# Kernel optimization log

Measured on AMD Instinct MI355X. Metric: run time of the kernel, lower is better.

Reference implementation:

```python
import jax, jax.numpy as jnp
import numpy as np

N_NODES = 100000
N_EDGES = 600000
HIDDEN = 128
BN_EPS = 1e-5


def setup_inputs() -> dict:
    key = jax.random.key(0)
    k_x, k_e, k_w, k_b, k_g = jax.random.split(key, 5)
    x = jax.random.normal(k_x, (N_NODES, HIDDEN), dtype=jnp.float32)
    edge_index = jax.random.randint(k_e, (2, N_EDGES), 0, N_NODES, dtype=jnp.int64)
    # GCNConv linear weight (no bias on the linear; bias added post-aggregation)
    scale = 1.0 / np.sqrt(HIDDEN)
    W = jax.random.uniform(k_w, (HIDDEN, HIDDEN), jnp.float32, -scale, scale)
    b = jax.random.uniform(k_b, (HIDDEN,), jnp.float32, -scale, scale)
    gamma = jnp.ones((HIDDEN,), jnp.float32)   # BatchNorm weight
    beta = jnp.zeros((HIDDEN,), jnp.float32)   # BatchNorm bias
    return {"x": x, "edge_index": edge_index, "W": W, "b": b, "gamma": gamma, "beta": beta}


def reference(x, edge_index, W, b, gamma, beta):
    N = x.shape[0]
    # ReLU then GCNConv linear transform: [N, D]
    h = jnp.matmul(jax.nn.relu(x), W)
    # Add self-loops (PyG GCNConv default)
    loops = jnp.arange(N, dtype=edge_index.dtype)
    row = jnp.concatenate([edge_index[0], loops])  # source nodes
    col = jnp.concatenate([edge_index[1], loops])  # target nodes
    # Symmetric normalization deg^{-1/2} with unit edge weights
    ones = jnp.ones(row.shape[0], dtype=h.dtype)
    deg = jax.ops.segment_sum(ones, col, num_segments=N)
    dinv = jnp.where(deg > 0, jax.lax.rsqrt(deg), 0.0)
    norm = dinv[row] * dinv[col]  # [E+N]
    # Gather -> scale -> scatter-add aggregation, then conv bias
    agg = jax.ops.segment_sum(norm[:, None] * h[row], col, num_segments=N)
    out = agg + b
    # BatchNorm1d (training mode: batch stats, biased variance)
    mean = jnp.mean(out, axis=0)
    var = jnp.var(out, axis=0)
    return gamma * (out - mean) * jax.lax.rsqrt(var + BN_EPS) + beta
```

## Files before the change

### kernel.cpp

```cpp
#include <hip/hip_runtime.h>

#define D 128
#define CAP 32
#define BN_EPS 1e-5f

typedef float floatx4 __attribute__((ext_vector_type(4)));
typedef __bf16 bf16x8 __attribute__((ext_vector_type(8)));

__device__ inline unsigned short f2bf(float f) {
    unsigned u; __builtin_memcpy(&u, &f, 4);
    unsigned r = (u + 0x7FFFu + ((u >> 16) & 1u)) >> 16;
    return (unsigned short)r;
}
__device__ inline float bflo(unsigned v) { unsigned x = v << 16; float f; __builtin_memcpy(&f, &x, 4); return f; }
__device__ inline float bfhi(unsigned v) { unsigned x = v & 0xFFFF0000u; float f; __builtin_memcpy(&f, &x, 4); return f; }

__global__ void setup_k(const unsigned* __restrict__ e, int* __restrict__ flag,
                        int* __restrict__ cursor, float* __restrict__ sums,
                        float* __restrict__ sumsq, const float* __restrict__ W,
                        unsigned short* __restrict__ Wt, int n_nodes) {
    int i = blockIdx.x * blockDim.x + threadIdx.x;
    if (i < n_nodes) cursor[i] = 0;
    if (i < D) { sums[i] = 0.f; sumsq[i] = 0.f; }
    if (i < D * D) {
        int n = i >> 7, k = i & 127;
        Wt[n * D + k] = f2bf(W[k * D + n]);
    }
    if (i == 0) {
        unsigned acc = 0;
        for (int k = 0; k < 64; ++k) acc |= e[2 * k + 1];
        *flag = (acc == 0u) ? 1 : 0;
    }
}

__global__ __launch_bounds__(256, 2) void gemm_k(const float* __restrict__ x,
                                                 const unsigned short* __restrict__ Wt,
                                                 unsigned short* __restrict__ h,
                                                 int n_mtiles) {
    int lane = threadIdx.x & 63;
    int wave = blockIdx.x * 4 + (threadIdx.x >> 6);
    int nw = gridDim.x * 4;
    int l15 = lane & 15;
    int quad = lane >> 4;

    bf16x8 Bf[4][8];
    for (int ks = 0; ks < 4; ++ks)
        for (int j = 0; j < 8; ++j)
            Bf[ks][j] = *(const bf16x8*)(Wt + (size_t)(j * 16 + l15) * D + ks * 32 + quad * 8);

    for (int mt = wave; mt < n_mtiles; mt += nw) {
        const float* xrow = x + (size_t)(mt * 16 + l15) * D + quad * 8;
        bf16x8 Af[4];
        for (int ks = 0; ks < 4; ++ks) {
            float4 a0 = *(const float4*)(xrow + ks * 32);
            float4 a1 = *(const float4*)(xrow + ks * 32 + 4);
            float av[8] = {a0.x, a0.y, a0.z, a0.w, a1.x, a1.y, a1.z, a1.w};
            union { unsigned short u[8]; bf16x8 v; } tmp;
            for (int jj = 0; jj < 8; ++jj) tmp.u[jj] = f2bf(fmaxf(av[jj], 0.0f));
            Af[ks] = tmp.v;
        }
        floatx4 acc[8];
        for (int j = 0; j < 8; ++j) acc[j] = (floatx4){0.f, 0.f, 0.f, 0.f};
        for (int ks = 0; ks < 4; ++ks)
            for (int j = 0; j < 8; ++j)
                acc[j] = __builtin_amdgcn_mfma_f32_16x16x32_bf16(Af[ks], Bf[ks][j], acc[j], 0, 0, 0);
        for (int j = 0; j < 8; ++j)
            for (int reg = 0; reg < 4; ++reg) {
                int rr = mt * 16 + quad * 4 + reg;
                int cc = j * 16 + l15;
                h[(size_t)rr * D + cc] = f2bf(acc[j][reg]);
            }
    }
}

__global__ __launch_bounds__(256) void bucket_k(const void* __restrict__ ep, const int* __restrict__ flag,
                                                int* __restrict__ cursor, int* __restrict__ bucket,
                                                int n_edges) {
    int e = blockIdx.x * blockDim.x + threadIdx.x;
    if (e >= n_edges) return;
    int r, c;
    if (*flag) {
        const long long* p = (const long long*)ep;
        r = (int)p[e]; c = (int)p[e + n_edges];
    } else {
        const int* p = (const int*)ep;
        r = p[e]; c = p[e + n_edges];
    }
    int pos = atomicAdd(&cursor[c], 1);
    if (pos < CAP) bucket[(size_t)c * CAP + pos] = r;
}

__global__ void dinv_k(const int* __restrict__ cursor, float* __restrict__ dinv, int n_nodes) {
    int i = blockIdx.x * blockDim.x + threadIdx.x;
    if (i < n_nodes) dinv[i] = rsqrtf(1.0f + (float)cursor[i]);
}

#define PREPD(s, rr) { int r_ = ((s) < degc) ? (rr) : node;              \
                       w##s = ((s) < degc) ? dinv[r_] : 0.0f;            \
                       hv##s = hp[(unsigned)r_ * 64u + lane]; }
#define ACC(s) { ax += w##s * bflo(hv##s); ay += w##s * bfhi(hv##s); }

__global__ __launch_bounds__(256) void agg_k(const unsigned short* __restrict__ h,
                                             const int* __restrict__ bucket,
                                             const int* __restrict__ cursor,
                                             const float* __restrict__ dinv,
                                             unsigned* __restrict__ aggb,
                                             int n_nodes) {
    int lane = threadIdx.x & 63;
    int node = blockIdx.x * 4 + (threadIdx.x >> 6);
    if (node >= n_nodes) return;
    const unsigned* hp = (const unsigned*)h;

    int deg = cursor[node];
    int degc = deg < CAP ? deg : CAP;
    float dc = dinv[node];

    unsigned v = hp[(unsigned)node * 64u + lane];
    float ax = dc * bflo(v), ay = dc * bfhi(v);
    const int* bk = bucket + (size_t)node * CAP;

    float w0=0,w1=0,w2=0,w3=0,w4=0,w5=0,w6=0,w7=0;
    unsigned hv0=0,hv1=0,hv2=0,hv3=0,hv4=0,hv5=0,hv6=0,hv7=0;

    if (degc > 0) { int4 b = *(const int4*)(bk);     PREPD(0,b.x) PREPD(1,b.y) PREPD(2,b.z) PREPD(3,b.w) }
    if (degc > 4) { int4 b = *(const int4*)(bk + 4); PREPD(4,b.x) PREPD(5,b.y) PREPD(6,b.z) PREPD(7,b.w) }

    if (degc <= 8) {
        ACC(0) ACC(1) ACC(2) ACC(3) ACC(4) ACC(5) ACC(6) ACC(7)
    } else {
        float w8=0,w9=0,w10=0,w11=0,w12=0,w13=0,w14=0,w15=0;
        unsigned hv8=0,hv9=0,hv10=0,hv11=0,hv12=0,hv13=0,hv14=0,hv15=0;
        { int4 b = *(const int4*)(bk + 8); PREPD(8,b.x) PREPD(9,b.y) PREPD(10,b.z) PREPD(11,b.w) }
        if (degc > 12) { int4 b = *(const int4*)(bk + 12); PREPD(12,b.x) PREPD(13,b.y) PREPD(14,b.z) PREPD(15,b.w) }
        ACC(0)  ACC(1)  ACC(2)  ACC(3)  ACC(4)  ACC(5)  ACC(6)  ACC(7)
        ACC(8)  ACC(9)  ACC(10) ACC(11) ACC(12) ACC(13) ACC(14) ACC(15)
        for (int e = 16; e < degc; ++e) {
            int r = bk[e];
            float dr = dinv[r];
            unsigned hh = hp[(unsigned)r * 64u + lane];
            ax += dr * bflo(hh); ay += dr * bfhi(hh);
        }
    }

    float ox = dc * ax, oy = dc * ay;
    aggb[(unsigned)node * 64u + lane] = ((unsigned)f2bf(oy) << 16) | (unsigned)f2bf(ox);
}

__global__ __launch_bounds__(256) void stats_k(const unsigned* __restrict__ aggb,
                                               float* __restrict__ sums, float* __restrict__ sumsq,
                                               int n_nodes) {
    __shared__ float red[256];
    int lane = threadIdx.x & 63;
    int wib = threadIdx.x >> 6;
    int wave = blockIdx.x * 4 + wib;
    int nw = gridDim.x * 4;
    float s0 = 0.f, s1 = 0.f, q0 = 0.f, q1 = 0.f;
    int n = wave;
    for (; n + 3 * nw < n_nodes; n += 4 * nw) {
        unsigned p0 = aggb[(size_t)n * 64 + lane];
        unsigned p1 = aggb[(size_t)(n + nw) * 64 + lane];
        unsigned p2 = aggb[(size_t)(n + 2 * nw) * 64 + lane];
        unsigned p3 = aggb[(size_t)(n + 3 * nw) * 64 + lane];
        float a0 = bflo(p0), b0 = bfhi(p0), a1 = bflo(p1), b1 = bfhi(p1);
        float a2 = bflo(p2), b2 = bfhi(p2), a3 = bflo(p3), b3 = bfhi(p3);
        s0 += a0 + a1 + a2 + a3;
        s1 += b0 + b1 + b2 + b3;
        q0 += a0 * a0 + a1 * a1 + a2 * a2 + a3 * a3;
        q1 += b0 * b0 + b1 * b1 + b2 * b2 + b3 * b3;
    }
    for (; n < n_nodes; n += nw) {
        unsigned p = aggb[(size_t)n * 64 + lane];
        float vx = bflo(p), vy = bfhi(p);
        s0 += vx; s1 += vy; q0 += vx * vx; q1 += vy * vy;
    }
    red[threadIdx.x] = s0; __syncthreads();
    if (wib == 0) atomicAdd(&sums[2 * lane], red[lane] + red[64 + lane] + red[128 + lane] + red[192 + lane]);
    __syncthreads();
    red[threadIdx.x] = s1; __syncthreads();
    if (wib == 0) atomicAdd(&sums[2 * lane + 1], red[lane] + red[64 + lane] + red[128 + lane] + red[192 + lane]);
    __syncthreads();
    red[threadIdx.x] = q0; __syncthreads();
    if (wib == 0) atomicAdd(&sumsq[2 * lane], red[lane] + red[64 + lane] + red[128 + lane] + red[192 + lane]);
    __syncthreads();
    red[threadIdx.x] = q1; __syncthreads();
    if (wib == 0) atomicAdd(&sumsq[2 * lane + 1], red[lane] + red[64 + lane] + red[128 + lane] + red[192 + lane]);
}

__global__ __launch_bounds__(256) void final_k(const unsigned* __restrict__ aggb,
                                               const float* __restrict__ sums, const float* __restrict__ sumsq,
                                               const float* __restrict__ gamma, const float* __restrict__ beta,
                                               float* __restrict__ out, int total4, float inv_n) {
    int i = blockIdx.x * blockDim.x + threadIdx.x;
    if (i >= total4) return;
    int idx = i * 4;
    int f = idx & (D - 1);
    float4 sm = *(const float4*)(sums + f);
    float4 sq = *(const float4*)(sumsq + f);
    float4 g  = *(const float4*)(gamma + f);
    float4 bt = *(const float4*)(beta + f);
    uint2 p = *(const uint2*)(aggb + i * 2);

    float m0 = sm.x * inv_n, m1 = sm.y * inv_n, m2 = sm.z * inv_n, m3 = sm.w * inv_n;
    float sc0 = g.x * rsqrtf(sq.x * inv_n - m0 * m0 + BN_EPS);
    float sc1 = g.y * rsqrtf(sq.y * inv_n - m1 * m1 + BN_EPS);
    float sc2 = g.z * rsqrtf(sq.z * inv_n - m2 * m2 + BN_EPS);
    float sc3 = g.w * rsqrtf(sq.w * inv_n - m3 * m3 + BN_EPS);
    float4 o;
    o.x = fmaf(bflo(p.x), sc0, bt.x - m0 * sc0);
    o.y = fmaf(bfhi(p.x), sc1, bt.y - m1 * sc1);
    o.z = fmaf(bflo(p.y), sc2, bt.z - m2 * sc2);
    o.w = fmaf(bfhi(p.y), sc3, bt.w - m3 * sc3);
    *(float4*)(out + idx) = o;
}

extern "C" void kernel_launch(void* const* d_in, const int* in_sizes, int n_in,
                              void* d_out, int out_size, void* d_ws, size_t ws_size,
                              hipStream_t stream) {
    const float* x     = (const float*)d_in[0];
    const void*  edges = d_in[1];
    const float* W     = (const float*)d_in[2];
    const float* gamma = (const float*)d_in[4];
    const float* beta  = (const float*)d_in[5];
    float* out = (float*)d_out;

    int N = in_sizes[0] / D;
    int E = in_sizes[1] / 2;

    char* ws = (char*)d_ws;
    size_t off = 0;
    auto alloc = [&](size_t bytes) { void* p = ws + off; off += (bytes + 255) & ~(size_t)255; return p; };
    unsigned short* h  = (unsigned short*)alloc((size_t)N * D * 2);
    unsigned* aggb     = (unsigned*)alloc((size_t)N * D * 2);
    int* bucket        = (int*)alloc((size_t)N * CAP * 4);
    int* cursor        = (int*)alloc((size_t)N * 4);
    float* dinv        = (float*)alloc((size_t)N * 4);
    unsigned short* Wt = (unsigned short*)alloc((size_t)D * D * 2);
    float* sums        = (float*)alloc(512);
    float* sumsq       = (float*)alloc(512);
    int* flag          = (int*)alloc(16);

    int nblk = (N + 255) / 256;
    int n_mtiles = N / 16;

    setup_k<<<nblk, 256, 0, stream>>>((const unsigned*)edges, flag, cursor, sums, sumsq, W, Wt, N);
    gemm_k<<<1563, 256, 0, stream>>>(x, Wt, h, n_mtiles);
    bucket_k<<<(E + 255) / 256, 256, 0, stream>>>(edges, flag, cursor, bucket, E);
    dinv_k<<<nblk, 256, 0, stream>>>(cursor, dinv, N);
    agg_k<<<(N + 3) / 4, 256, 0, stream>>>(h, bucket, cursor, dinv, aggb, N);
    stats_k<<<512, 256, 0, stream>>>(aggb, sums, sumsq, N);
    final_k<<<(N * D / 4 + 255) / 256, 256, 0, stream>>>(aggb, sums, sumsq, gamma, beta, out, N * D / 4, 1.0f / (float)N);
}
```

Baseline: 251.9 us.

## Fuse GEMM with edge bucketing, fold degree norm and BN stats into aggregation

Merges the GEMM and edge-bucketing kernels into one launch, with every fourth group of blocks doing atomic bucketing while the rest run MFMA tiles, so the two overlap. Drops the dinv kernel and computes rsqrt of the degree inline from cursor inside aggregation. Aggregation becomes a persistent grid-stride kernel that also accumulates per-block BatchNorm sums into a partials buffer, which a small second kernel reduces. This removes the separate stats pass that re-read aggb. The cost is redundant rsqrt and cursor loads per neighbor, plus a fixed block-to-role split.

```diff
diff --git a/kernel.cpp b/kernel.cpp
--- a/kernel.cpp
+++ b/kernel.cpp
@@ -33,13 +33,44 @@
     }
 }
 
-__global__ __launch_bounds__(256, 2) void gemm_k(const float* __restrict__ x,
-                                                 const unsigned short* __restrict__ Wt,
-                                                 unsigned short* __restrict__ h,
-                                                 int n_mtiles) {
+__global__ __launch_bounds__(256, 2) void gb_k(const float* __restrict__ x,
+                                               const unsigned short* __restrict__ Wt,
+                                               unsigned short* __restrict__ h,
+                                               int n_mtiles,
+                                               const void* __restrict__ ep,
+                                               const int* __restrict__ flag,
+                                               int* __restrict__ cursor,
+                                               int* __restrict__ bucket,
+                                               int n_edges) {
+    int b = blockIdx.x;
+    int g = b >> 3;
+    int ngroups = (int)gridDim.x >> 3;
+    int nbg = ngroups >> 2;
+
+    if ((g & 3) == 3) {
+        int bb = (g >> 2) * 8 + (b & 7);
+        int stride = nbg * 8 * 256;
+        int fl = *flag;
+        for (int e = bb * 256 + (int)threadIdx.x; e < n_edges; e += stride) {
+            int r, c;
+            if (fl) {
+                const long long* p = (const long long*)ep;
+                r = (int)p[e]; c = (int)p[e + n_edges];
+            } else {
+                const int* p = (const int*)ep;
+                r = p[e]; c = p[e + n_edges];
+            }
+            int pos = atomicAdd(&cursor[c], 1);
+            if (pos < CAP) bucket[(size_t)c * CAP + pos] = r;
+        }
+        return;
+    }
+
+    int gg = (g >> 2) * 3 + (g & 3);
+    int gb = gg * 8 + (b & 7);
     int lane = threadIdx.x & 63;
-    int wave = blockIdx.x * 4 + (threadIdx.x >> 6);
-    int nw = gridDim.x * 4;
+    int wave = gb * 4 + (threadIdx.x >> 6);
+    int nw = (ngroups - nbg) * 32;
     int l15 = lane & 15;
     int quad = lane >> 4;
 
@@ -73,117 +104,84 @@
     }
 }
 
-__global__ __launch_bounds__(256) void bucket_k(const void* __restrict__ ep, const int* __restrict__ flag,
-                                                int* __restrict__ cursor, int* __restrict__ bucket,
-                                                int n_edges) {
-    int e = blockIdx.x * blockDim.x + threadIdx.x;
-    if (e >= n_edges) return;
-    int r, c;
-    if (*flag) {
-        const long long* p = (const long long*)ep;
-        r = (int)p[e]; c = (int)p[e + n_edges];
-    } else {
-        const int* p = (const int*)ep;
-        r = p[e]; c = p[e + n_edges];
-    }
-    int pos = atomicAdd(&cursor[c], 1);
-    if (pos < CAP) bucket[(size_t)c * CAP + pos] = r;
-}
-
-__global__ void dinv_k(const int* __restrict__ cursor, float* __restrict__ dinv, int n_nodes) {
-    int i = blockIdx.x * blockDim.x + threadIdx.x;
-    if (i < n_nodes) dinv[i] = rsqrtf(1.0f + (float)cursor[i]);
-}
-
-#define PREPD(s, rr) { int r_ = ((s) < degc) ? (rr) : node;              \
-                       w##s = ((s) < degc) ? dinv[r_] : 0.0f;            \
+#define PREPD(s, rr) { int r_ = ((s) < degc) ? (rr) : node;                         \
+                       float cd_ = (float)cursor[r_];                                \
+                       w##s = ((s) < degc) ? rsqrtf(1.0f + cd_) : 0.0f;              \
                        hv##s = hp[(unsigned)r_ * 64u + lane]; }
 #define ACC(s) { ax += w##s * bflo(hv##s); ay += w##s * bfhi(hv##s); }
 
 __global__ __launch_bounds__(256) void agg_k(const unsigned short* __restrict__ h,
                                              const int* __restrict__ bucket,
                                              const int* __restrict__ cursor,
-                                             const float* __restrict__ dinv,
                                              unsigned* __restrict__ aggb,
+                                             float* __restrict__ partials,
                                              int n_nodes) {
-    int lane = threadIdx.x & 63;
-    int node = blockIdx.x * 4 + (threadIdx.x >> 6);
-    if (node >= n_nodes) return;
-    const unsigned* hp = (const unsigned*)h;
-
-    int deg = cursor[node];
-    int degc = deg < CAP ? deg : CAP;
-    float dc = dinv[node];
-
-    unsigned v = hp[(unsigned)node * 64u + lane];
-    float ax = dc * bflo(v), ay = dc * bfhi(v);
-    const int* bk = bucket + (size_t)node * CAP;
-
-    float w0=0,w1=0,w2=0,w3=0,w4=0,w5=0,w6=0,w7=0;
-    unsigned hv0=0,hv1=0,hv2=0,hv3=0,hv4=0,hv5=0,hv6=0,hv7=0;
-
-    if (degc > 0) { int4 b = *(const int4*)(bk);     PREPD(0,b.x) PREPD(1,b.y) PREPD(2,b.z) PREPD(3,b.w) }
-    if (degc > 4) { int4 b = *(const int4*)(bk + 4); PREPD(4,b.x) PREPD(5,b.y) PREPD(6,b.z) PREPD(7,b.w) }
-
-    if (degc <= 8) {
-        ACC(0) ACC(1) ACC(2) ACC(3) ACC(4) ACC(5) ACC(6) ACC(7)
-    } else {
-        float w8=0,w9=0,w10=0,w11=0,w12=0,w13=0,w14=0,w15=0;
-        unsigned hv8=0,hv9=0,hv10=0,hv11=0,hv12=0,hv13=0,hv14=0,hv15=0;
-        { int4 b = *(const int4*)(bk + 8); PREPD(8,b.x) PREPD(9,b.y) PREPD(10,b.z) PREPD(11,b.w) }
-        if (degc > 12) { int4 b = *(const int4*)(bk + 12); PREPD(12,b.x) PREPD(13,b.y) PREPD(14,b.z) PREPD(15,b.w) }
-        ACC(0)  ACC(1)  ACC(2)  ACC(3)  ACC(4)  ACC(5)  ACC(6)  ACC(7)
-        ACC(8)  ACC(9)  ACC(10) ACC(11) ACC(12) ACC(13) ACC(14) ACC(15)
-        for (int e = 16; e < degc; ++e) {
-            int r = bk[e];
-            float dr = dinv[r];
-            unsigned hh = hp[(unsigned)r * 64u + lane];
-            ax += dr * bflo(hh); ay += dr * bfhi(hh);
-        }
-    }
-
-    float ox = dc * ax, oy = dc * ay;
-    aggb[(unsigned)node * 64u + lane] = ((unsigned)f2bf(oy) << 16) | (unsigned)f2bf(ox);
-}
-
-__global__ __launch_bounds__(256) void stats_k(const unsigned* __restrict__ aggb,
-                                               float* __restrict__ sums, float* __restrict__ sumsq,
-                                               int n_nodes) {
     __shared__ float red[256];
     int lane = threadIdx.x & 63;
     int wib = threadIdx.x >> 6;
-    int wave = blockIdx.x * 4 + wib;
     int nw = gridDim.x * 4;
+    const unsigned* hp = (const unsigned*)h;
     float s0 = 0.f, s1 = 0.f, q0 = 0.f, q1 = 0.f;
-    int n = wave;
-    for (; n + 3 * nw < n_nodes; n += 4 * nw) {
-        unsigned p0 = aggb[(size_t)n * 64 + lane];
-        unsigned p1 = aggb[(size_t)(n + nw) * 64 + lane];
-        unsigned p2 = aggb[(size_t)(n + 2 * nw) * 64 + lane];
-        unsigned p3 = aggb[(size_t)(n + 3 * nw) * 64 + lane];
-        float a0 = bflo(p0), b0 = bfhi(p0), a1 = bflo(p1), b1 = bfhi(p1);
-        float a2 = bflo(p2), b2 = bfhi(p2), a3 = bflo(p3), b3 = bfhi(p3);
-        s0 += a0 + a1 + a2 + a3;
-        s1 += b0 + b1 + b2 + b3;
-        q0 += a0 * a0 + a1 * a1 + a2 * a2 + a3 * a3;
-        q1 += b0 * b0 + b1 * b1 + b2 * b2 + b3 * b3;
-    }
-    for (; n < n_nodes; n += nw) {
-        unsigned p = aggb[(size_t)n * 64 + lane];
-        float vx = bflo(p), vy = bfhi(p);
-        s0 += vx; s1 += vy; q0 += vx * vx; q1 += vy * vy;
-    }
+
+    for (int node = blockIdx.x * 4 + wib; node < n_nodes; node += nw) {
+        int deg = cursor[node];
+        int degc = deg < CAP ? deg : CAP;
+        float dc = rsqrtf(1.0f + (float)deg);
+
+        unsigned v = hp[(unsigned)node * 64u + lane];
+        float ax = dc * bflo(v), ay = dc * bfhi(v);
+        const int* bk = bucket + (size_t)node * CAP;
+
+        float w0=0,w1=0,w2=0,w3=0,w4=0,w5=0,w6=0,w7=0;
+        unsigned hv0=0,hv1=0,hv2=0,hv3=0,hv4=0,hv5=0,hv6=0,hv7=0;
+
+        if (degc > 0) { int4 b4 = *(const int4*)(bk);     PREPD(0,b4.x) PREPD(1,b4.y) PREPD(2,b4.z) PREPD(3,b4.w) }
+        if (degc > 4) { int4 b4 = *(const int4*)(bk + 4); PREPD(4,b4.x) PREPD(5,b4.y) PREPD(6,b4.z) PREPD(7,b4.w) }
+
+        if (degc <= 8) {
+            ACC(0) ACC(1) ACC(2) ACC(3) ACC(4) ACC(5) ACC(6) ACC(7)
+        } else {
+            float w8=0,w9=0,w10=0,w11=0,w12=0,w13=0,w14=0,w15=0;
+            unsigned hv8=0,hv9=0,hv10=0,hv11=0,hv12=0,hv13=0,hv14=0,hv15=0;
+            { int4 b4 = *(const int4*)(bk + 8); PREPD(8,b4.x) PREPD(9,b4.y) PREPD(10,b4.z) PREPD(11,b4.w) }
+            if (degc > 12) { int4 b4 = *(const int4*)(bk + 12); PREPD(12,b4.x) PREPD(13,b4.y) PREPD(14,b4.z) PREPD(15,b4.w) }
+            ACC(0)  ACC(1)  ACC(2)  ACC(3)  ACC(4)  ACC(5)  ACC(6)  ACC(7)
+            ACC(8)  ACC(9)  ACC(10) ACC(11) ACC(12) ACC(13) ACC(14) ACC(15)
+            for (int e = 16; e < degc; ++e) {
+                int r = bk[e];
+                float dr = rsqrtf(1.0f + (float)cursor[r]);
+                unsigned hh = hp[(unsigned)r * 64u + lane];
+                ax += dr * bflo(hh); ay += dr * bfhi(hh);
+            }
+        }
+
+        float ox = dc * ax, oy = dc * ay;
+        unsigned pk = ((unsigned)f2bf(oy) << 16) | (unsigned)f2bf(ox);
+        __builtin_nontemporal_store(pk, &aggb[(unsigned)node * 64u + lane]);
+        s0 += ox; s1 += oy; q0 += ox * ox; q1 += oy * oy;
+    }
+
+    float* pb = partials + (size_t)blockIdx.x * 256;
     red[threadIdx.x] = s0; __syncthreads();
-    if (wib == 0) atomicAdd(&sums[2 * lane], red[lane] + red[64 + lane] + red[128 + lane] + red[192 + lane]);
-    __syncthreads();
-    red[threadIdx.x] = s1; __syncthreads();
-    if (wib == 0) atomicAdd(&sums[2 * lane + 1], red[lane] + red[64 + lane] + red[128 + lane] + red[192 + lane]);
-    __syncthreads();
-    red[threadIdx.x] = q0; __syncthreads();
-    if (wib == 0) atomicAdd(&sumsq[2 * lane], red[lane] + red[64 + lane] + red[128 + lane] + red[192 + lane]);
-    __syncthreads();
-    red[threadIdx.x] = q1; __syncthreads();
-    if (wib == 0) atomicAdd(&sumsq[2 * lane + 1], red[lane] + red[64 + lane] + red[128 + lane] + red[192 + lane]);
+    if (wib == 0) pb[2 * lane]       = red[lane] + red[64 + lane] + red[128 + lane] + red[192 + lane];
+    __syncthreads(); red[threadIdx.x] = s1; __syncthreads();
+    if (wib == 0) pb[2 * lane + 1]   = red[lane] + red[64 + lane] + red[128 + lane] + red[192 + lane];
+    __syncthreads(); red[threadIdx.x] = q0; __syncthreads();
+    if (wib == 0) pb[128 + 2 * lane] = red[lane] + red[64 + lane] + red[128 + lane] + red[192 + lane];
+    __syncthreads(); red[threadIdx.x] = q1; __syncthreads();
+    if (wib == 0) pb[129 + 2 * lane] = red[lane] + red[64 + lane] + red[128 + lane] + red[192 + lane];
+}
+
+__global__ __launch_bounds__(256) void stats2_k(const float* __restrict__ partials,
+                                                float* __restrict__ sums, float* __restrict__ sumsq,
+                                                int nblk) {
+    int tid = threadIdx.x;
+    int per = nblk / gridDim.x;
+    int b0 = blockIdx.x * per;
+    float acc = 0.f;
+    for (int bb = b0; bb < b0 + per; ++bb) acc += partials[(size_t)bb * 256 + tid];
+    if (tid < 128) atomicAdd(&sums[tid], acc);
+    else           atomicAdd(&sumsq[tid - 128], acc);
 }
 
 __global__ __launch_bounds__(256) void final_k(const unsigned* __restrict__ aggb,
@@ -233,8 +231,8 @@
     unsigned* aggb     = (unsigned*)alloc((size_t)N * D * 2);
     int* bucket        = (int*)alloc((size_t)N * CAP * 4);
     int* cursor        = (int*)alloc((size_t)N * 4);
-    float* dinv        = (float*)alloc((size_t)N * 4);
     unsigned short* Wt = (unsigned short*)alloc((size_t)D * D * 2);
+    float* partials    = (float*)alloc((size_t)2048 * 256 * 4);
     float* sums        = (float*)alloc(512);
     float* sumsq       = (float*)alloc(512);
     int* flag          = (int*)alloc(16);
@@ -243,10 +241,8 @@
     int n_mtiles = N / 16;
 
     setup_k<<<nblk, 256, 0, stream>>>((const unsigned*)edges, flag, cursor, sums, sumsq, W, Wt, N);
-    gemm_k<<<1563, 256, 0, stream>>>(x, Wt, h, n_mtiles);
-    bucket_k<<<(E + 255) / 256, 256, 0, stream>>>(edges, flag, cursor, bucket, E);
-    dinv_k<<<nblk, 256, 0, stream>>>(cursor, dinv, N);
-    agg_k<<<(N + 3) / 4, 256, 0, stream>>>(h, bucket, cursor, dinv, aggb, N);
-    stats_k<<<512, 256, 0, stream>>>(aggb, sums, sumsq, N);
+    gb_k<<<2080, 256, 0, stream>>>(x, Wt, h, n_mtiles, edges, flag, cursor, bucket, E);
+    agg_k<<<2048, 256, 0, stream>>>(h, bucket, cursor, aggb, partials, N);
+    stats2_k<<<32, 256, 0, stream>>>(partials, sums, sumsq, 2048);
     final_k<<<(N * D / 4 + 255) / 256, 256, 0, stream>>>(aggb, sums, sumsq, gamma, beta, out, N * D / 4, 1.0f / (float)N);
 }
```

Result: slower. 260.8 us (+3.6%).

## Fuse GEMM and edge bucketing into one kernel with block-role partitioning

Applied to the files above, without the earlier changes.

Merges the dense ReLU-GEMM kernel and the edge-bucketing atomic kernel into a single launch. Every fourth group of 8 blocks is assigned to bucketing with a grid-stride loop over the edges, and the remaining blocks run the GEMM over the row tiles. The memory-bound GEMM and the atomic-heavy scatter can then overlap on the GPU, and one launch and its inter-kernel gap go away. In exchange, fewer blocks are left for the GEMM, and the two workloads compete for bandwidth.

```diff
diff --git a/kernel.cpp b/kernel.cpp
--- a/kernel.cpp
+++ b/kernel.cpp
@@ -33,13 +33,44 @@
     }
 }
 
-__global__ __launch_bounds__(256, 2) void gemm_k(const float* __restrict__ x,
-                                                 const unsigned short* __restrict__ Wt,
-                                                 unsigned short* __restrict__ h,
-                                                 int n_mtiles) {
+__global__ __launch_bounds__(256, 2) void gb_k(const float* __restrict__ x,
+                                               const unsigned short* __restrict__ Wt,
+                                               unsigned short* __restrict__ h,
+                                               int n_mtiles,
+                                               const void* __restrict__ ep,
+                                               const int* __restrict__ flag,
+                                               int* __restrict__ cursor,
+                                               int* __restrict__ bucket,
+                                               int n_edges) {
+    int b = blockIdx.x;
+    int g = b >> 3;
+    int ngroups = (int)gridDim.x >> 3;
+    int nbg = ngroups >> 2;
+
+    if ((g & 3) == 3) {
+        int bb = (g >> 2) * 8 + (b & 7);
+        int stride = nbg * 8 * 256;
+        int fl = *flag;
+        for (int e = bb * 256 + (int)threadIdx.x; e < n_edges; e += stride) {
+            int r, c;
+            if (fl) {
+                const long long* p = (const long long*)ep;
+                r = (int)p[e]; c = (int)p[e + n_edges];
+            } else {
+                const int* p = (const int*)ep;
+                r = p[e]; c = p[e + n_edges];
+            }
+            int pos = atomicAdd(&cursor[c], 1);
+            if (pos < CAP) bucket[(size_t)c * CAP + pos] = r;
+        }
+        return;
+    }
+
+    int gg = (g >> 2) * 3 + (g & 3);
+    int gb = gg * 8 + (b & 7);
     int lane = threadIdx.x & 63;
-    int wave = blockIdx.x * 4 + (threadIdx.x >> 6);
-    int nw = gridDim.x * 4;
+    int wave = gb * 4 + (threadIdx.x >> 6);
+    int nw = (ngroups - nbg) * 32;
     int l15 = lane & 15;
     int quad = lane >> 4;
 
@@ -73,23 +104,6 @@
     }
 }
 
-__global__ __launch_bounds__(256) void bucket_k(const void* __restrict__ ep, const int* __restrict__ flag,
-                                                int* __restrict__ cursor, int* __restrict__ bucket,
-                                                int n_edges) {
-    int e = blockIdx.x * blockDim.x + threadIdx.x;
-    if (e >= n_edges) return;
-    int r, c;
-    if (*flag) {
-        const long long* p = (const long long*)ep;
-        r = (int)p[e]; c = (int)p[e + n_edges];
-    } else {
-        const int* p = (const int*)ep;
-        r = p[e]; c = p[e + n_edges];
-    }
-    int pos = atomicAdd(&cursor[c], 1);
-    if (pos < CAP) bucket[(size_t)c * CAP + pos] = r;
-}
-
 __global__ void dinv_k(const int* __restrict__ cursor, float* __restrict__ dinv, int n_nodes) {
     int i = blockIdx.x * blockDim.x + threadIdx.x;
     if (i < n_nodes) dinv[i] = rsqrtf(1.0f + (float)cursor[i]);
@@ -243,8 +257,7 @@
     int n_mtiles = N / 16;
 
     setup_k<<<nblk, 256, 0, stream>>>((const unsigned*)edges, flag, cursor, sums, sumsq, W, Wt, N);
-    gemm_k<<<1563, 256, 0, stream>>>(x, Wt, h, n_mtiles);
-    bucket_k<<<(E + 255) / 256, 256, 0, stream>>>(edges, flag, cursor, bucket, E);
+    gb_k<<<2080, 256, 0, stream>>>(x, Wt, h, n_mtiles, edges, flag, cursor, bucket, E);
     dinv_k<<<nblk, 256, 0, stream>>>(cursor, dinv, N);
     agg_k<<<(N + 3) / 4, 256, 0, stream>>>(h, bucket, cursor, dinv, aggb, N);
     stats_k<<<512, 256, 0, stream>>>(aggb, sums, sumsq, N);
```

Measured after the change: 230.2 us. 8.6% less time.

## Fuse all stages into one cooperative persistent kernel with grid syncs

Applied to the files above, without the earlier changes.

Replaces the seven separate launches with a single cooperative kernel that runs setup, edge bucketing plus GEMM, dinv, aggregation, BN stats and the final normalize, separated by grid.sync barriers. The bucketing and the GEMM now run concurrently on disjoint block groups (3/8 and 5/8 of the grid), overlapping the atomic scatter with the MFMA work. The aim is to remove launch gaps and overlap independent stages. The cost is grid-wide barrier overhead, a persistent grid capped at 2048 blocks with grid-stride loops, and higher register pressure from the 4-blocks-per-CU launch bound.

```diff
diff --git a/kernel.cpp b/kernel.cpp
--- a/kernel.cpp
+++ b/kernel.cpp
@@ -1,4 +1,7 @@
 #include <hip/hip_runtime.h>
+#include <hip/hip_cooperative_groups.h>
+
+namespace cg = cooperative_groups;
 
 #define D 128
 #define CAP 32
@@ -15,202 +18,206 @@
 __device__ inline float bflo(unsigned v) { unsigned x = v << 16; float f; __builtin_memcpy(&f, &x, 4); return f; }
 __device__ inline float bfhi(unsigned v) { unsigned x = v & 0xFFFF0000u; float f; __builtin_memcpy(&f, &x, 4); return f; }
 
-__global__ void setup_k(const unsigned* __restrict__ e, int* __restrict__ flag,
-                        int* __restrict__ cursor, float* __restrict__ sums,
-                        float* __restrict__ sumsq, const float* __restrict__ W,
-                        unsigned short* __restrict__ Wt, int n_nodes) {
-    int i = blockIdx.x * blockDim.x + threadIdx.x;
-    if (i < n_nodes) cursor[i] = 0;
-    if (i < D) { sums[i] = 0.f; sumsq[i] = 0.f; }
-    if (i < D * D) {
-        int n = i >> 7, k = i & 127;
-        Wt[n * D + k] = f2bf(W[k * D + n]);
-    }
-    if (i == 0) {
-        unsigned acc = 0;
-        for (int k = 0; k < 64; ++k) acc |= e[2 * k + 1];
-        *flag = (acc == 0u) ? 1 : 0;
-    }
-}
-
-__global__ __launch_bounds__(256, 2) void gemm_k(const float* __restrict__ x,
-                                                 const unsigned short* __restrict__ Wt,
-                                                 unsigned short* __restrict__ h,
-                                                 int n_mtiles) {
-    int lane = threadIdx.x & 63;
-    int wave = blockIdx.x * 4 + (threadIdx.x >> 6);
-    int nw = gridDim.x * 4;
-    int l15 = lane & 15;
-    int quad = lane >> 4;
-
-    bf16x8 Bf[4][8];
-    for (int ks = 0; ks < 4; ++ks)
-        for (int j = 0; j < 8; ++j)
-            Bf[ks][j] = *(const bf16x8*)(Wt + (size_t)(j * 16 + l15) * D + ks * 32 + quad * 8);
-
-    for (int mt = wave; mt < n_mtiles; mt += nw) {
-        const float* xrow = x + (size_t)(mt * 16 + l15) * D + quad * 8;
-        bf16x8 Af[4];
-        for (int ks = 0; ks < 4; ++ks) {
-            float4 a0 = *(const float4*)(xrow + ks * 32);
-            float4 a1 = *(const float4*)(xrow + ks * 32 + 4);
-            float av[8] = {a0.x, a0.y, a0.z, a0.w, a1.x, a1.y, a1.z, a1.w};
-            union { unsigned short u[8]; bf16x8 v; } tmp;
-            for (int jj = 0; jj < 8; ++jj) tmp.u[jj] = f2bf(fmaxf(av[jj], 0.0f));
-            Af[ks] = tmp.v;
-        }
-        floatx4 acc[8];
-        for (int j = 0; j < 8; ++j) acc[j] = (floatx4){0.f, 0.f, 0.f, 0.f};
-        for (int ks = 0; ks < 4; ++ks)
-            for (int j = 0; j < 8; ++j)
-                acc[j] = __builtin_amdgcn_mfma_f32_16x16x32_bf16(Af[ks], Bf[ks][j], acc[j], 0, 0, 0);
-        for (int j = 0; j < 8; ++j)
-            for (int reg = 0; reg < 4; ++reg) {
-                int rr = mt * 16 + quad * 4 + reg;
-                int cc = j * 16 + l15;
-                h[(size_t)rr * D + cc] = f2bf(acc[j][reg]);
-            }
-    }
-}
-
-__global__ __launch_bounds__(256) void bucket_k(const void* __restrict__ ep, const int* __restrict__ flag,
-                                                int* __restrict__ cursor, int* __restrict__ bucket,
-                                                int n_edges) {
-    int e = blockIdx.x * blockDim.x + threadIdx.x;
-    if (e >= n_edges) return;
-    int r, c;
-    if (*flag) {
-        const long long* p = (const long long*)ep;
-        r = (int)p[e]; c = (int)p[e + n_edges];
-    } else {
-        const int* p = (const int*)ep;
-        r = p[e]; c = p[e + n_edges];
-    }
-    int pos = atomicAdd(&cursor[c], 1);
-    if (pos < CAP) bucket[(size_t)c * CAP + pos] = r;
-}
-
-__global__ void dinv_k(const int* __restrict__ cursor, float* __restrict__ dinv, int n_nodes) {
-    int i = blockIdx.x * blockDim.x + threadIdx.x;
-    if (i < n_nodes) dinv[i] = rsqrtf(1.0f + (float)cursor[i]);
-}
-
 #define PREPD(s, rr) { int r_ = ((s) < degc) ? (rr) : node;              \
                        w##s = ((s) < degc) ? dinv[r_] : 0.0f;            \
                        hv##s = hp[(unsigned)r_ * 64u + lane]; }
 #define ACC(s) { ax += w##s * bflo(hv##s); ay += w##s * bfhi(hv##s); }
 
-__global__ __launch_bounds__(256) void agg_k(const unsigned short* __restrict__ h,
-                                             const int* __restrict__ bucket,
-                                             const int* __restrict__ cursor,
-                                             const float* __restrict__ dinv,
-                                             unsigned* __restrict__ aggb,
-                                             int n_nodes) {
-    int lane = threadIdx.x & 63;
-    int node = blockIdx.x * 4 + (threadIdx.x >> 6);
-    if (node >= n_nodes) return;
-    const unsigned* hp = (const unsigned*)h;
-
-    int deg = cursor[node];
-    int degc = deg < CAP ? deg : CAP;
-    float dc = dinv[node];
-
-    unsigned v = hp[(unsigned)node * 64u + lane];
-    float ax = dc * bflo(v), ay = dc * bfhi(v);
-    const int* bk = bucket + (size_t)node * CAP;
-
-    float w0=0,w1=0,w2=0,w3=0,w4=0,w5=0,w6=0,w7=0;
-    unsigned hv0=0,hv1=0,hv2=0,hv3=0,hv4=0,hv5=0,hv6=0,hv7=0;
-
-    if (degc > 0) { int4 b = *(const int4*)(bk);     PREPD(0,b.x) PREPD(1,b.y) PREPD(2,b.z) PREPD(3,b.w) }
-    if (degc > 4) { int4 b = *(const int4*)(bk + 4); PREPD(4,b.x) PREPD(5,b.y) PREPD(6,b.z) PREPD(7,b.w) }
-
-    if (degc <= 8) {
-        ACC(0) ACC(1) ACC(2) ACC(3) ACC(4) ACC(5) ACC(6) ACC(7)
-    } else {
-        float w8=0,w9=0,w10=0,w11=0,w12=0,w13=0,w14=0,w15=0;
-        unsigned hv8=0,hv9=0,hv10=0,hv11=0,hv12=0,hv13=0,hv14=0,hv15=0;
-        { int4 b = *(const int4*)(bk + 8); PREPD(8,b.x) PREPD(9,b.y) PREPD(10,b.z) PREPD(11,b.w) }
-        if (degc > 12) { int4 b = *(const int4*)(bk + 12); PREPD(12,b.x) PREPD(13,b.y) PREPD(14,b.z) PREPD(15,b.w) }
-        ACC(0)  ACC(1)  ACC(2)  ACC(3)  ACC(4)  ACC(5)  ACC(6)  ACC(7)
-        ACC(8)  ACC(9)  ACC(10) ACC(11) ACC(12) ACC(13) ACC(14) ACC(15)
-        for (int e = 16; e < degc; ++e) {
-            int r = bk[e];
-            float dr = dinv[r];
-            unsigned hh = hp[(unsigned)r * 64u + lane];
-            ax += dr * bflo(hh); ay += dr * bfhi(hh);
-        }
-    }
-
-    float ox = dc * ax, oy = dc * ay;
-    aggb[(unsigned)node * 64u + lane] = ((unsigned)f2bf(oy) << 16) | (unsigned)f2bf(ox);
-}
-
-__global__ __launch_bounds__(256) void stats_k(const unsigned* __restrict__ aggb,
-                                               float* __restrict__ sums, float* __restrict__ sumsq,
-                                               int n_nodes) {
+__global__ __launch_bounds__(256, 4) void mega_k(
+    const float* __restrict__ x, const void* __restrict__ ep,
+    const float* __restrict__ W, const float* __restrict__ gamma,
+    const float* __restrict__ beta, float* __restrict__ out,
+    unsigned short* __restrict__ h, unsigned* __restrict__ aggb,
+    int* __restrict__ bucket, int* __restrict__ cursor,
+    float* __restrict__ dinv, unsigned short* __restrict__ Wt,
+    float* __restrict__ sums, float* __restrict__ sumsq,
+    int* __restrict__ flag, int N, int E, int n_mtiles, float inv_n)
+{
+    cg::grid_group grid = cg::this_grid();
     __shared__ float red[256];
-    int lane = threadIdx.x & 63;
-    int wib = threadIdx.x >> 6;
-    int wave = blockIdx.x * 4 + wib;
-    int nw = gridDim.x * 4;
-    float s0 = 0.f, s1 = 0.f, q0 = 0.f, q1 = 0.f;
-    int n = wave;
-    for (; n + 3 * nw < n_nodes; n += 4 * nw) {
-        unsigned p0 = aggb[(size_t)n * 64 + lane];
-        unsigned p1 = aggb[(size_t)(n + nw) * 64 + lane];
-        unsigned p2 = aggb[(size_t)(n + 2 * nw) * 64 + lane];
-        unsigned p3 = aggb[(size_t)(n + 3 * nw) * 64 + lane];
-        float a0 = bflo(p0), b0 = bfhi(p0), a1 = bflo(p1), b1 = bfhi(p1);
-        float a2 = bflo(p2), b2 = bfhi(p2), a3 = bflo(p3), b3 = bfhi(p3);
-        s0 += a0 + a1 + a2 + a3;
-        s1 += b0 + b1 + b2 + b3;
-        q0 += a0 * a0 + a1 * a1 + a2 * a2 + a3 * a3;
-        q1 += b0 * b0 + b1 * b1 + b2 * b2 + b3 * b3;
-    }
-    for (; n < n_nodes; n += nw) {
-        unsigned p = aggb[(size_t)n * 64 + lane];
-        float vx = bflo(p), vy = bfhi(p);
-        s0 += vx; s1 += vy; q0 += vx * vx; q1 += vy * vy;
-    }
-    red[threadIdx.x] = s0; __syncthreads();
-    if (wib == 0) atomicAdd(&sums[2 * lane], red[lane] + red[64 + lane] + red[128 + lane] + red[192 + lane]);
-    __syncthreads();
-    red[threadIdx.x] = s1; __syncthreads();
-    if (wib == 0) atomicAdd(&sums[2 * lane + 1], red[lane] + red[64 + lane] + red[128 + lane] + red[192 + lane]);
-    __syncthreads();
-    red[threadIdx.x] = q0; __syncthreads();
-    if (wib == 0) atomicAdd(&sumsq[2 * lane], red[lane] + red[64 + lane] + red[128 + lane] + red[192 + lane]);
-    __syncthreads();
-    red[threadIdx.x] = q1; __syncthreads();
-    if (wib == 0) atomicAdd(&sumsq[2 * lane + 1], red[lane] + red[64 + lane] + red[128 + lane] + red[192 + lane]);
-}
-
-__global__ __launch_bounds__(256) void final_k(const unsigned* __restrict__ aggb,
-                                               const float* __restrict__ sums, const float* __restrict__ sumsq,
-                                               const float* __restrict__ gamma, const float* __restrict__ beta,
-                                               float* __restrict__ out, int total4, float inv_n) {
-    int i = blockIdx.x * blockDim.x + threadIdx.x;
-    if (i >= total4) return;
-    int idx = i * 4;
-    int f = idx & (D - 1);
-    float4 sm = *(const float4*)(sums + f);
-    float4 sq = *(const float4*)(sumsq + f);
-    float4 g  = *(const float4*)(gamma + f);
-    float4 bt = *(const float4*)(beta + f);
-    uint2 p = *(const uint2*)(aggb + i * 2);
-
-    float m0 = sm.x * inv_n, m1 = sm.y * inv_n, m2 = sm.z * inv_n, m3 = sm.w * inv_n;
-    float sc0 = g.x * rsqrtf(sq.x * inv_n - m0 * m0 + BN_EPS);
-    float sc1 = g.y * rsqrtf(sq.y * inv_n - m1 * m1 + BN_EPS);
-    float sc2 = g.z * rsqrtf(sq.z * inv_n - m2 * m2 + BN_EPS);
-    float sc3 = g.w * rsqrtf(sq.w * inv_n - m3 * m3 + BN_EPS);
-    float4 o;
-    o.x = fmaf(bflo(p.x), sc0, bt.x - m0 * sc0);
-    o.y = fmaf(bfhi(p.x), sc1, bt.y - m1 * sc1);
-    o.z = fmaf(bflo(p.y), sc2, bt.z - m2 * sc2);
-    o.w = fmaf(bfhi(p.y), sc3, bt.w - m3 * sc3);
-    *(float4*)(out + idx) = o;
+    const int tid  = blockIdx.x * 256 + (int)threadIdx.x;
+    const int nth  = (int)gridDim.x * 256;
+    const int lane = threadIdx.x & 63;
+    const int wib  = threadIdx.x >> 6;
+
+    for (int i = tid; i < N; i += nth) cursor[i] = 0;
+    if (tid < D * D) {
+        int n = tid >> 7, k = tid & 127;
+        Wt[n * D + k] = f2bf(W[k * D + n]);
+    }
+    if (tid < D) { sums[tid] = 0.f; sumsq[tid] = 0.f; }
+    if (tid == 0) {
+        const unsigned* e = (const unsigned*)ep;
+        unsigned acc = 0;
+        for (int k = 0; k < 64; ++k) acc |= e[2 * k + 1];
+        *flag = (acc == 0u) ? 1 : 0;
+    }
+    grid.sync();
+
+    {
+        int b = blockIdx.x;
+        int g = b >> 3;
+        int noct = (int)gridDim.x >> 6;
+        if ((g & 7) < 3) {
+            int bb = (g >> 3) * 3 + (g & 7);
+            int t  = (bb * 8 + (b & 7)) * 256 + (int)threadIdx.x;
+            int nt = noct * 3 * 8 * 256;
+            int fl = *flag;
+            for (int e = t; e < E; e += nt) {
+                int r, c;
+                if (fl) {
+                    const long long* p = (const long long*)ep;
+                    r = (int)p[e]; c = (int)p[e + E];
+                } else {
+                    const int* p = (const int*)ep;
+                    r = p[e]; c = p[e + E];
+                }
+                int pos = atomicAdd(&cursor[c], 1);
+                if (pos < CAP) bucket[(size_t)c * CAP + pos] = r;
+            }
+        } else {
+            int gg   = (g >> 3) * 5 + ((g & 7) - 3);
+            int gb   = gg * 8 + (b & 7);
+            int wave = gb * 4 + wib;
+            int nw   = noct * 5 * 8 * 4;
+            int l15  = lane & 15;
+            int quad = lane >> 4;
+
+            bf16x8 Bf[4][8];
+            for (int ks = 0; ks < 4; ++ks)
+                for (int j = 0; j < 8; ++j)
+                    Bf[ks][j] = *(const bf16x8*)(Wt + (size_t)(j * 16 + l15) * D + ks * 32 + quad * 8);
+
+            for (int mt = wave; mt < n_mtiles; mt += nw) {
+                const float* xrow = x + (size_t)(mt * 16 + l15) * D + quad * 8;
+                bf16x8 Af[4];
+                for (int ks = 0; ks < 4; ++ks) {
+                    float4 a0 = *(const float4*)(xrow + ks * 32);
+                    float4 a1 = *(const float4*)(xrow + ks * 32 + 4);
+                    float av[8] = {a0.x, a0.y, a0.z, a0.w, a1.x, a1.y, a1.z, a1.w};
+                    union { unsigned short u[8]; bf16x8 v; } tmp;
+                    for (int jj = 0; jj < 8; ++jj) tmp.u[jj] = f2bf(fmaxf(av[jj], 0.0f));
+                    Af[ks] = tmp.v;
+                }
+                floatx4 acc[8];
+                for (int j = 0; j < 8; ++j) acc[j] = (floatx4){0.f, 0.f, 0.f, 0.f};
+                for (int ks = 0; ks < 4; ++ks)
+                    for (int j = 0; j < 8; ++j)
+                        acc[j] = __builtin_amdgcn_mfma_f32_16x16x32_bf16(Af[ks], Bf[ks][j], acc[j], 0, 0, 0);
+                for (int j = 0; j < 8; ++j)
+                    for (int reg = 0; reg < 4; ++reg) {
+                        int rr = mt * 16 + quad * 4 + reg;
+                        int cc = j * 16 + l15;
+                        h[(size_t)rr * D + cc] = f2bf(acc[j][reg]);
+                    }
+            }
+        }
+    }
+    grid.sync();
+
+    for (int i = tid; i < N; i += nth) dinv[i] = rsqrtf(1.0f + (float)cursor[i]);
+    grid.sync();
+
+    {
+        const unsigned* hp = (const unsigned*)h;
+        int nwav = (int)gridDim.x * 4;
+        for (int node = blockIdx.x * 4 + wib; node < N; node += nwav) {
+            int deg = cursor[node];
+            int degc = deg < CAP ? deg : CAP;
+            float dc = dinv[node];
+
+            unsigned v = hp[(unsigned)node * 64u + lane];
+            float ax = dc * bflo(v), ay = dc * bfhi(v);
+            const int* bk = bucket + (size_t)node * CAP;
+
+            float w0=0,w1=0,w2=0,w3=0,w4=0,w5=0,w6=0,w7=0;
+            unsigned hv0=0,hv1=0,hv2=0,hv3=0,hv4=0,hv5=0,hv6=0,hv7=0;
+
+            if (degc > 0) { int4 b4 = *(const int4*)(bk);     PREPD(0,b4.x) PREPD(1,b4.y) PREPD(2,b4.z) PREPD(3,b4.w) }
+            if (degc > 4) { int4 b4 = *(const int4*)(bk + 4); PREPD(4,b4.x) PREPD(5,b4.y) PREPD(6,b4.z) PREPD(7,b4.w) }
+
+            if (degc <= 8) {
+                ACC(0) ACC(1) ACC(2) ACC(3) ACC(4) ACC(5) ACC(6) ACC(7)
+            } else {
+                float w8=0,w9=0,w10=0,w11=0,w12=0,w13=0,w14=0,w15=0;
+                unsigned hv8=0,hv9=0,hv10=0,hv11=0,hv12=0,hv13=0,hv14=0,hv15=0;
+                { int4 b4 = *(const int4*)(bk + 8); PREPD(8,b4.x) PREPD(9,b4.y) PREPD(10,b4.z) PREPD(11,b4.w) }
+                if (degc > 12) { int4 b4 = *(const int4*)(bk + 12); PREPD(12,b4.x) PREPD(13,b4.y) PREPD(14,b4.z) PREPD(15,b4.w) }
+                ACC(0)  ACC(1)  ACC(2)  ACC(3)  ACC(4)  ACC(5)  ACC(6)  ACC(7)
+                ACC(8)  ACC(9)  ACC(10) ACC(11) ACC(12) ACC(13) ACC(14) ACC(15)
+                for (int e = 16; e < degc; ++e) {
+                    int r = bk[e];
+                    float dr = dinv[r];
+                    unsigned hh = hp[(unsigned)r * 64u + lane];
+                    ax += dr * bflo(hh); ay += dr * bfhi(hh);
+                }
+            }
+
+            float ox = dc * ax, oy = dc * ay;
+            aggb[(unsigned)node * 64u + lane] = ((unsigned)f2bf(oy) << 16) | (unsigned)f2bf(ox);
+        }
+    }
+    grid.sync();
+
+    {
+        int nw = (int)gridDim.x * 4;
+        float s0 = 0.f, s1 = 0.f, q0 = 0.f, q1 = 0.f;
+        int n = blockIdx.x * 4 + wib;
+        for (; n + 3 * nw < N; n += 4 * nw) {
+            unsigned p0 = aggb[(size_t)n * 64 + lane];
+            unsigned p1 = aggb[(size_t)(n + nw) * 64 + lane];
+            unsigned p2 = aggb[(size_t)(n + 2 * nw) * 64 + lane];
+            unsigned p3 = aggb[(size_t)(n + 3 * nw) * 64 + lane];
+            float a0 = bflo(p0), b0 = bfhi(p0), a1 = bflo(p1), b1 = bfhi(p1);
+            float a2 = bflo(p2), b2 = bfhi(p2), a3 = bflo(p3), b3 = bfhi(p3);
+            s0 += a0 + a1 + a2 + a3;
+            s1 += b0 + b1 + b2 + b3;
+            q0 += a0 * a0 + a1 * a1 + a2 * a2 + a3 * a3;
+            q1 += b0 * b0 + b1 * b1 + b2 * b2 + b3 * b3;
+        }
+        for (; n < N; n += nw) {
+            unsigned p = aggb[(size_t)n * 64 + lane];
+            float vx = bflo(p), vy = bfhi(p);
+            s0 += vx; s1 += vy; q0 += vx * vx; q1 += vy * vy;
+        }
+        red[threadIdx.x] = s0; __syncthreads();
+        if (wib == 0) atomicAdd(&sums[2 * lane], red[lane] + red[64 + lane] + red[128 + lane] + red[192 + lane]);
+        __syncthreads();
+        red[threadIdx.x] = s1; __syncthreads();
+        if (wib == 0) atomicAdd(&sums[2 * lane + 1], red[lane] + red[64 + lane] + red[128 + lane] + red[192 + lane]);
+        __syncthreads();
+        red[threadIdx.x] = q0; __syncthreads();
+        if (wib == 0) atomicAdd(&sumsq[2 * lane], red[lane] + red[64 + lane] + red[128 + lane] + red[192 + lane]);
+        __syncthreads();
+        red[threadIdx.x] = q1; __syncthreads();
+        if (wib == 0) atomicAdd(&sumsq[2 * lane + 1], red[lane] + red[64 + lane] + red[128 + lane] + red[192 + lane]);
+    }
+    grid.sync();
+
+    {
+        int total4 = N * (D / 4);
+        for (int i = tid; i < total4; i += nth) {
+            int idx = i * 4;
+            int f = idx & (D - 1);
+            float4 sm = *(const float4*)(sums + f);
+            float4 sq = *(const float4*)(sumsq + f);
+            float4 gm = *(const float4*)(gamma + f);
+            float4 bt = *(const float4*)(beta + f);
+            uint2 p = *(const uint2*)(aggb + (size_t)i * 2);
+
+            float m0 = sm.x * inv_n, m1 = sm.y * inv_n, m2 = sm.z * inv_n, m3 = sm.w * inv_n;
+            float sc0 = gm.x * rsqrtf(sq.x * inv_n - m0 * m0 + BN_EPS);
+            float sc1 = gm.y * rsqrtf(sq.y * inv_n - m1 * m1 + BN_EPS);
+            float sc2 = gm.z * rsqrtf(sq.z * inv_n - m2 * m2 + BN_EPS);
+            float sc3 = gm.w * rsqrtf(sq.w * inv_n - m3 * m3 + BN_EPS);
+            float4 o;
+            o.x = fmaf(bflo(p.x), sc0, bt.x - m0 * sc0);
+            o.y = fmaf(bfhi(p.x), sc1, bt.y - m1 * sc1);
+            o.z = fmaf(bflo(p.y), sc2, bt.z - m2 * sc2);
+            o.w = fmaf(bfhi(p.y), sc3, bt.w - m3 * sc3);
+            *(float4*)(out + idx) = o;
+        }
+    }
 }
 
 extern "C" void kernel_launch(void* const* d_in, const int* in_sizes, int n_in,
@@ -239,14 +246,20 @@
     float* sumsq       = (float*)alloc(512);
     int* flag          = (int*)alloc(16);
 
-    int nblk = (N + 255) / 256;
     int n_mtiles = N / 16;
-
-    setup_k<<<nblk, 256, 0, stream>>>((const unsigned*)edges, flag, cursor, sums, sumsq, W, Wt, N);
-    gemm_k<<<1563, 256, 0, stream>>>(x, Wt, h, n_mtiles);
-    bucket_k<<<(E + 255) / 256, 256, 0, stream>>>(edges, flag, cursor, bucket, E);
-    dinv_k<<<nblk, 256, 0, stream>>>(cursor, dinv, N);
-    agg_k<<<(N + 3) / 4, 256, 0, stream>>>(h, bucket, cursor, dinv, aggb, N);
-    stats_k<<<512, 256, 0, stream>>>(aggb, sums, sumsq, N);
-    final_k<<<(N * D / 4 + 255) / 256, 256, 0, stream>>>(aggb, sums, sumsq, gamma, beta, out, N * D / 4, 1.0f / (float)N);
+    float inv_n = 1.0f / (float)N;
+
+    int maxb = 0;
+    hipOccupancyMaxActiveBlocksPerMultiprocessor(&maxb, mega_k, 256, 0);
+    if (maxb < 1) maxb = 1;
+    int grid = maxb * 256;
+    if (grid > 2048) grid = 2048;
+    grid &= ~63;
+    if (grid < 64) grid = 64;
+
+    void* args[] = { (void*)&x, (void*)&edges, (void*)&W, (void*)&gamma, (void*)&beta,
+                     (void*)&out, (void*)&h, (void*)&aggb, (void*)&bucket, (void*)&cursor,
+                     (void*)&dinv, (void*)&Wt, (void*)&sums, (void*)&sumsq, (void*)&flag,
+                     (void*)&N, (void*)&E, (void*)&n_mtiles, (void*)&inv_n };
+    hipLaunchCooperativeKernel((const void*)mega_k, dim3(grid), dim3(256), args, 0, stream);
 }
```

Result: slower. 557.7 us (+121.4%).
